# Performance work log

Hardware: AMD Instinct MI355X
Metric: run time of the kernel (lower is better)

The kernel has to match this reference:

```python
import jax, jax.numpy as jnp
import numpy as np

N_NODES = 100000
N_EDGES = 1600000
N_FEAT = 128
N_HID = 128


def cheb_conv_k2(x, edge_index, W0, W1, b):
    """PyG ChebConv with K=2, sym norm, lambda_max=2.0.
    Reduces to: out = x @ W0 + (L_hat x) @ W1 + b, where
    L_hat = 2L/lambda_max - I = -D^{-1/2} A D^{-1/2} (diagonal cancels).
    """
    n = x.shape[0]
    row, col = edge_index[0], edge_index[1]
    deg = jax.ops.segment_sum(jnp.ones_like(row, dtype=x.dtype), row, num_segments=n)
    dinv = jnp.where(deg > 0, jax.lax.rsqrt(jnp.maximum(deg, 1.0)), 0.0)
    w = -(dinv[row] * dinv[col])                     # [E] edge weights of L_hat
    tx1 = jax.ops.segment_sum(x[col] * w[:, None], row, num_segments=n)  # [N, F]
    return x @ W0 + tx1 @ W1 + b


def setup_inputs() -> dict:
    key = jax.random.key(0)
    ks = jax.random.split(key, 8)
    glorot = lambda k, fi, fo: jax.random.normal(k, (fi, fo), dtype=jnp.float32) * np.float32(np.sqrt(2.0 / (fi + fo)))
    x = jax.random.normal(ks[0], (N_NODES, N_FEAT), dtype=jnp.float32)
    edge_index = jax.random.randint(ks[1], (2, N_EDGES), 0, N_NODES, dtype=jnp.int64 if jax.config.jax_enable_x64 else jnp.int32)
    return {
        "x": x,
        "edge_index": edge_index,
        "W0_1": glorot(ks[2], N_FEAT, N_HID),
        "W1_1": glorot(ks[3], N_FEAT, N_HID),
        "b1": jnp.zeros((N_HID,), dtype=jnp.float32),
        "W0_2": glorot(ks[4], N_HID, N_HID),
        "W1_2": glorot(ks[5], N_HID, N_HID),
        "b2": jnp.zeros((N_HID,), dtype=jnp.float32),
    }


def reference(x, edge_index, W0_1, W1_1, b1, W0_2, W1_2, b2):
    # eval mode: input Dropout, dropout_adj(p=0.8), and per-layer Dropout are identity
    x1 = jax.nn.relu(cheb_conv_k2(x, edge_index, W0_1, W1_1, b1))
    x2 = jax.nn.relu(cheb_conv_k2(x1, edge_index, W0_2, W1_2, b2))
    # mean of the two layer outputs; outAct is identity
    return (x1 + x2) * 0.5
```

## Files before the change

### kernel.cpp

```cpp
#include <hip/hip_runtime.h>

#define NN 100000
#define NE 1600000
#define NF 128
#define NSTRIP2 (NN / 32)
#define NBUCK ((NN + 127) / 128)
#define CAP 2560
#define CHUNK 4096

typedef __attribute__((ext_vector_type(8))) short short8;
typedef __attribute__((ext_vector_type(4))) float f32x4;

__device__ __forceinline__ unsigned short f2b(float f) {
    union { float f; unsigned int u; } v; v.f = f;
    unsigned int u = v.u;
    unsigned int r = (u + 0x7fffu + ((u >> 16) & 1u)) >> 16;
    return (unsigned short)r;
}

__global__ __launch_bounds__(256) void k_bin(const int* __restrict__ row,
                                             const int* __restrict__ col,
                                             int* __restrict__ gcur,
                                             unsigned int* __restrict__ gslab) {
    __shared__ int hist[NBUCK];
    __shared__ int start[NBUCK];
    __shared__ int gbase[NBUCK];
    __shared__ int scanbuf[256];
    __shared__ unsigned int stage[CHUNK];
    __shared__ unsigned short sb[CHUNK];

    const int t = threadIdx.x;
    const int e0 = blockIdx.x * CHUNK;
    const int cnt = min(CHUNK, NE - e0);

    for (int i = t; i < NBUCK; i += 256) hist[i] = 0;
    __syncthreads();
    for (int i = t; i < cnt; i += 256) atomicAdd(&hist[row[e0 + i] >> 7], 1);
    __syncthreads();

    const int b0 = t * 4;
    int s = 0;
#pragma unroll
    for (int k = 0; k < 4; ++k) { int idx = b0 + k; if (idx < NBUCK) s += hist[idx]; }
    scanbuf[t] = s;
    __syncthreads();
    for (int off = 1; off < 256; off <<= 1) {
        int u = t >= off ? scanbuf[t - off] : 0;
        __syncthreads();
        scanbuf[t] += u;
        __syncthreads();
    }
    int run = t > 0 ? scanbuf[t - 1] : 0;
#pragma unroll
    for (int k = 0; k < 4; ++k) {
        int idx = b0 + k;
        if (idx < NBUCK) { start[idx] = run; run += hist[idx]; }
    }
    __syncthreads();

    for (int i = t; i < NBUCK; i += 256) {
        int c = hist[i];
        gbase[i] = c > 0 ? atomicAdd(&gcur[i], c) : 0;
        hist[i] = start[i];
    }
    __syncthreads();

    for (int i = t; i < cnt; i += 256) {
        int r = row[e0 + i];
        int b = r >> 7;
        int p = atomicAdd(&hist[b], 1);
        stage[p] = (unsigned int)col[e0 + i] | ((unsigned int)(r & 127) << 17);
        sb[p] = (unsigned short)b;
    }
    __syncthreads();

    for (int i = t; i < cnt; i += 256) {
        int b = sb[i];
        gslab[gbase[b] + (i - start[b])] = stage[i];
    }
}

__global__ __launch_bounds__(256) void k_bscan(const int* __restrict__ gcur,
                                               int* __restrict__ bbase) {
    __shared__ int s[NBUCK];
    int t = threadIdx.x;
    for (int i = t; i < NBUCK; i += 256) s[i] = gcur[i] - i * CAP;
    __syncthreads();
    if (t == 0) {
        int run = 0;
        for (int i = 0; i < NBUCK; ++i) { int v = s[i]; s[i] = run; run += v; }
    }
    __syncthreads();
    for (int i = t; i < NBUCK; i += 256) bbase[i] = s[i];
}

__global__ __launch_bounds__(256) void k_csr(const unsigned int* __restrict__ gslab,
                                             const int* __restrict__ gcur,
                                             const int* __restrict__ bbase,
                                             int* __restrict__ offs,
                                             int* __restrict__ ccol,
                                             float* __restrict__ dinv) {
    __shared__ int rh[128];
    __shared__ int rcur[128];
    __shared__ unsigned int scol[CAP];

    const int b = blockIdx.x;
    const int segbase = b * CAP;
    const int cnt = gcur[b] - segbase;
    const int csr0 = bbase[b];
    const int t = threadIdx.x;

    if (t < 128) rh[t] = 0;
    __syncthreads();
    for (int i = t; i < cnt; i += 256) atomicAdd(&rh[gslab[segbase + i] >> 17], 1);
    __syncthreads();
    if (t == 0) {
        int run = 0;
        for (int r = 0; r < 128; ++r) { rcur[r] = run; run += rh[r]; }
    }
    __syncthreads();

    const int rbase = b * 128;
    if (t < 128 && rbase + t < NN) {
        offs[rbase + t] = csr0 + rcur[t];
        int d = rh[t];
        dinv[rbase + t] = d > 0 ? rsqrtf((float)d) : 0.0f;
    }
    if (b == NBUCK - 1 && t == 0) offs[NN] = NE;
    __syncthreads();

    for (int i = t; i < cnt; i += 256) {
        unsigned int v = gslab[segbase + i];
        int p = atomicAdd(&rcur[v >> 17], 1);
        scol[p] = v & 0x1ffff;
    }
    __syncthreads();
    for (int i = t; i < cnt; i += 256) ccol[csr0 + i] = scol[i];
}

__global__ __launch_bounds__(256) void k_quant(const float* __restrict__ x,
                                               const float* __restrict__ dinv,
                                               unsigned short* __restrict__ xq,
                                               float* __restrict__ dsc,
                                               float* __restrict__ sx) {
    int r = (blockIdx.x * 256 + threadIdx.x) >> 6;
    int lane = threadIdx.x & 63;
    float2 v = ((const float2*)x)[r * 64 + lane];
    float m = fmaxf(fabsf(v.x), fabsf(v.y));
#pragma unroll
    for (int mask = 32; mask; mask >>= 1) m = fmaxf(m, __shfl_xor(m, mask));
    float s = m * (1.0f / 127.0f);
    float inv = m > 0.0f ? 127.0f / m : 0.0f;
    int qx = (int)rintf(v.x * inv) + 128;
    int qy = (int)rintf(v.y * inv) + 128;
    xq[r * 64 + lane] = (unsigned short)(qx | (qy << 8));
    if (lane == 0) { dsc[r] = dinv[r] * s; sx[r] = s; }
}

__global__ __launch_bounds__(256) void k_pack(const float* __restrict__ W01,
                                              const float* __restrict__ W11,
                                              const float* __restrict__ W02,
                                              const float* __restrict__ W12,
                                              unsigned short* __restrict__ WP,
                                              int* __restrict__ gcur) {
    int idx = blockIdx.x * 256 + threadIdx.x;
    if (idx < NBUCK) gcur[idx] = idx * CAP;
    int mi = idx >> 14;
    int e = idx & 16383;
    const float* W = mi == 0 ? W01 : mi == 1 ? W02 : mi == 2 ? W11 : W12;
    int midx = mi == 0 ? 0 : mi == 1 ? 2 : mi == 2 ? 1 : 3;
    int k = e >> 7, n = e & 127;
    int kt = k >> 5, g = (k >> 3) & 3, j = k & 7;
    WP[midx * 16384 + (((kt * 4 + g) * 128 + n) << 3) + j] = f2b(W[e]);
}

__global__ __launch_bounds__(256) void k_gather(const int* __restrict__ offs,
                                                const int* __restrict__ ccol,
                                                const float* __restrict__ dsc,
                                                const float* __restrict__ dinv,
                                                const uint2* __restrict__ xq64,
                                                uint2* __restrict__ txq8,
                                                float* __restrict__ st_out,
                                                float qbias) {
    int r = (blockIdx.x * 256 + threadIdx.x) >> 6;
    if (r >= NN) return;
    int lane = threadIdx.x & 63;
    int fl = lane & 15, q = lane >> 4;
    int beg = offs[r], end = offs[r + 1];
    float a0 = 0.f, a1 = 0.f, a2 = 0.f, a3 = 0.f;
    float a4 = 0.f, a5 = 0.f, a6 = 0.f, a7 = 0.f, S = 0.f;
    int j = beg + q;
    for (; j + 12 < end; j += 16) {
        int c0 = ccol[j], c1 = ccol[j + 4], c2 = ccol[j + 8], c3 = ccol[j + 12];
        float w0 = dsc[c0], w1 = dsc[c1], w2 = dsc[c2], w3 = dsc[c3];
        uint2 u0 = xq64[c0 * 16 + fl];
        uint2 u1 = xq64[c1 * 16 + fl];
        uint2 u2 = xq64[c2 * 16 + fl];
        uint2 u3 = xq64[c3 * 16 + fl];
        a0 += w0 * (float)(u0.x & 0xffu)         + w1 * (float)(u1.x & 0xffu)
            + w2 * (float)(u2.x & 0xffu)         + w3 * (float)(u3.x & 0xffu);
        a1 += w0 * (float)((u0.x >> 8) & 0xffu)  + w1 * (float)((u1.x >> 8) & 0xffu)
            + w2 * (float)((u2.x >> 8) & 0xffu)  + w3 * (float)((u3.x >> 8) & 0xffu);
        a2 += w0 * (float)((u0.x >> 16) & 0xffu) + w1 * (float)((u1.x >> 16) & 0xffu)
            + w2 * (float)((u2.x >> 16) & 0xffu) + w3 * (float)((u3.x >> 16) & 0xffu);
        a3 += w0 * (float)(u0.x >> 24)           + w1 * (float)(u1.x >> 24)
            + w2 * (float)(u2.x >> 24)           + w3 * (float)(u3.x >> 24);
        a4 += w0 * (float)(u0.y & 0xffu)         + w1 * (float)(u1.y & 0xffu)
            + w2 * (float)(u2.y & 0xffu)         + w3 * (float)(u3.y & 0xffu);
        a5 += w0 * (float)((u0.y >> 8) & 0xffu)  + w1 * (float)((u1.y >> 8) & 0xffu)
            + w2 * (float)((u2.y >> 8) & 0xffu)  + w3 * (float)((u3.y >> 8) & 0xffu);
        a6 += w0 * (float)((u0.y >> 16) & 0xffu) + w1 * (float)((u1.y >> 16) & 0xffu)
            + w2 * (float)((u2.y >> 16) & 0xffu) + w3 * (float)((u3.y >> 16) & 0xffu);
        a7 += w0 * (float)(u0.y >> 24)           + w1 * (float)(u1.y >> 24)
            + w2 * (float)(u2.y >> 24)           + w3 * (float)(u3.y >> 24);
        S += w0 + w1 + w2 + w3;
    }
    for (; j < end; j += 4) {
        int c = ccol[j];
        float w = dsc[c];
        uint2 u = xq64[c * 16 + fl];
        a0 += w * (float)(u.x & 0xffu);
        a1 += w * (float)((u.x >> 8) & 0xffu);
        a2 += w * (float)((u.x >> 16) & 0xffu);
        a3 += w * (float)(u.x >> 24);
        a4 += w * (float)(u.y & 0xffu);
        a5 += w * (float)((u.y >> 8) & 0xffu);
        a6 += w * (float)((u.y >> 16) & 0xffu);
        a7 += w * (float)(u.y >> 24);
        S += w;
    }
#pragma unroll
    for (int mask = 32; mask >= 16; mask >>= 1) {
        a0 += __shfl_xor(a0, mask); a1 += __shfl_xor(a1, mask);
        a2 += __shfl_xor(a2, mask); a3 += __shfl_xor(a3, mask);
        a4 += __shfl_xor(a4, mask); a5 += __shfl_xor(a5, mask);
        a6 += __shfl_xor(a6, mask); a7 += __shfl_xor(a7, mask);
        S  += __shfl_xor(S, mask);
    }
    if (q == 0) {
        float s = -dinv[r];
        float qb = qbias * S;
        a0 = s * (a0 - qb); a1 = s * (a1 - qb); a2 = s * (a2 - qb); a3 = s * (a3 - qb);
        a4 = s * (a4 - qb); a5 = s * (a5 - qb); a6 = s * (a6 - qb); a7 = s * (a7 - qb);
        float mx = fmaxf(fmaxf(fmaxf(fabsf(a0), fabsf(a1)), fmaxf(fabsf(a2), fabsf(a3))),
                         fmaxf(fmaxf(fabsf(a4), fabsf(a5)), fmaxf(fabsf(a6), fabsf(a7))));
#pragma unroll
        for (int mask = 8; mask; mask >>= 1) mx = fmaxf(mx, __shfl_xor(mx, mask));
        float st = mx * (1.0f / 127.0f);
        float invt = mx > 0.0f ? 127.0f / mx : 0.0f;
        int q0 = (int)rintf(a0 * invt) + 128, q1 = (int)rintf(a1 * invt) + 128;
        int q2 = (int)rintf(a2 * invt) + 128, q3 = (int)rintf(a3 * invt) + 128;
        int q4 = (int)rintf(a4 * invt) + 128, q5 = (int)rintf(a5 * invt) + 128;
        int q6 = (int)rintf(a6 * invt) + 128, q7 = (int)rintf(a7 * invt) + 128;
        uint2 o;
        o.x = (unsigned)q0 | ((unsigned)q1 << 8) | ((unsigned)q2 << 16) | ((unsigned)q3 << 24);
        o.y = (unsigned)q4 | ((unsigned)q5 << 8) | ((unsigned)q6 << 16) | ((unsigned)q7 << 24);
        txq8[r * 16 + fl] = o;
        if (fl == 0) st_out[r] = st;
    }
}

__global__ __launch_bounds__(256) void k_mm(const unsigned char* __restrict__ Aq,
                                            const float* __restrict__ s_in,
                                            float qoff,
                                            const unsigned char* __restrict__ Tq8,
                                            const float* __restrict__ st_in,
                                            const unsigned short* __restrict__ WP0,
                                            const unsigned short* __restrict__ WP1,
                                            const float* __restrict__ bias,
                                            const float* __restrict__ dinv,
                                            float* __restrict__ out,
                                            unsigned char* __restrict__ Qout,
                                            float* __restrict__ dsc_out,
                                            float* __restrict__ s1_out,
                                            int mode) {
    int wid = (blockIdx.x * 256 + threadIdx.x) >> 6;
    if (wid >= NSTRIP2) return;
    int lane = threadIdx.x & 63;
    int g = lane >> 4, m = lane & 15;

    short8 a[2][4], t[2][4];
#pragma unroll
    for (int s = 0; s < 2; ++s) {
        int row = wid * 32 + s * 16 + m;
        float sA = s_in[row];
        float sT = st_in[row];
        const unsigned char* Arow = Aq + (size_t)row * NF + g * 8;
        const unsigned char* Trow = Tq8 + (size_t)row * NF + g * 8;
#pragma unroll
        for (int kt = 0; kt < 4; ++kt) {
            uint2 u = *(const uint2*)(Arow + kt * 32);
            short8 v;
            v[0] = f2b(sA * ((float)(u.x & 0xffu) - qoff));
            v[1] = f2b(sA * ((float)((u.x >> 8) & 0xffu) - qoff));
            v[2] = f2b(sA * ((float)((u.x >> 16) & 0xffu) - qoff));
            v[3] = f2b(sA * ((float)(u.x >> 24) - qoff));
            v[4] = f2b(sA * ((float)(u.y & 0xffu) - qoff));
            v[5] = f2b(sA * ((float)((u.y >> 8) & 0xffu) - qoff));
            v[6] = f2b(sA * ((float)((u.y >> 16) & 0xffu) - qoff));
            v[7] = f2b(sA * ((float)(u.y >> 24) - qoff));
            a[s][kt] = v;
            uint2 w = *(const uint2*)(Trow + kt * 32);
            short8 tv;
            tv[0] = f2b(sT * ((float)(w.x & 0xffu) - 128.0f));
            tv[1] = f2b(sT * ((float)((w.x >> 8) & 0xffu) - 128.0f));
            tv[2] = f2b(sT * ((float)((w.x >> 16) & 0xffu) - 128.0f));
            tv[3] = f2b(sT * ((float)(w.x >> 24) - 128.0f));
            tv[4] = f2b(sT * ((float)(w.y & 0xffu) - 128.0f));
            tv[5] = f2b(sT * ((float)((w.y >> 8) & 0xffu) - 128.0f));
            tv[6] = f2b(sT * ((float)((w.y >> 16) & 0xffu) - 128.0f));
            tv[7] = f2b(sT * ((float)(w.y >> 24) - 128.0f));
            t[s][kt] = tv;
        }
    }

    const short8* B0 = (const short8*)WP0 + g * 128 + m;
    const short8* B1 = (const short8*)WP1 + g * 128 + m;

    f32x4 acc[2][8];
#pragma unroll
    for (int nt = 0; nt < 8; ++nt) {
        float b = bias[nt * 16 + m];
#pragma unroll
        for (int s = 0; s < 2; ++s) {
            acc[s][nt][0] = b; acc[s][nt][1] = b; acc[s][nt][2] = b; acc[s][nt][3] = b;
        }
    }

#pragma unroll
    for (int nt = 0; nt < 8; ++nt) {
#pragma unroll
        for (int kt = 0; kt < 4; ++kt) {
            short8 b0 = B0[kt * 512 + nt * 16];
            short8 b1 = B1[kt * 512 + nt * 16];
#pragma unroll
            for (int s = 0; s < 2; ++s) {
                acc[s][nt] = __builtin_amdgcn_mfma_f32_16x16x32_bf16(a[s][kt], b0, acc[s][nt], 0, 0, 0);
                acc[s][nt] = __builtin_amdgcn_mfma_f32_16x16x32_bf16(t[s][kt], b1, acc[s][nt], 0, 0, 0);
            }
        }
    }

#pragma unroll
    for (int s = 0; s < 2; ++s)
#pragma unroll
        for (int nt = 0; nt < 8; ++nt)
#pragma unroll
            for (int r = 0; r < 4; ++r) acc[s][nt][r] = fmaxf(acc[s][nt][r], 0.0f);

    if (mode == 0) {
#pragma unroll
        for (int s = 0; s < 2; ++s) {
            int rbase = wid * 32 + s * 16 + g * 4;
            float mr[4] = {0.0f, 0.0f, 0.0f, 0.0f};
#pragma unroll
            for (int nt = 0; nt < 8; ++nt)
#pragma unroll
                for (int r = 0; r < 4; ++r) mr[r] = fmaxf(mr[r], acc[s][nt][r]);
#pragma unroll
            for (int mask = 1; mask < 16; mask <<= 1)
#pragma unroll
                for (int r = 0; r < 4; ++r) mr[r] = fmaxf(mr[r], __shfl_xor(mr[r], mask));

            float inv[4], s1v[4];
#pragma unroll
            for (int r = 0; r < 4; ++r) {
                s1v[r] = mr[r] * (1.0f / 255.0f);
                inv[r] = mr[r] > 0.0f ? 255.0f / mr[r] : 0.0f;
            }
#pragma unroll
            for (int nt = 0; nt < 8; ++nt) {
                int c = nt * 16 + m;
#pragma unroll
                for (int r = 0; r < 4; ++r) {
                    int qv = (int)rintf(acc[s][nt][r] * inv[r]);
                    qv = qv > 255 ? 255 : qv;
                    Qout[(size_t)(rbase + r) * NF + c] = (unsigned char)qv;
                }
            }
            if (m == 0) {
#pragma unroll
                for (int r = 0; r < 4; ++r) {
                    s1_out[rbase + r] = s1v[r];
                    dsc_out[rbase + r] = dinv[rbase + r] * s1v[r];
                }
            }
        }
    } else {
#pragma unroll
        for (int s = 0; s < 2; ++s) {
            int rbase = wid * 32 + s * 16 + g * 4;
            float sR[4];
#pragma unroll
            for (int r = 0; r < 4; ++r) sR[r] = s_in[rbase + r];
#pragma unroll
            for (int nt = 0; nt < 8; ++nt) {
                int c = nt * 16 + m;
#pragma unroll
                for (int r = 0; r < 4; ++r) {
                    size_t o = (size_t)(rbase + r) * NF + c;
                    float x1v = sR[r] * (float)Aq[o];
                    out[o] = 0.5f * (x1v + acc[s][nt][r]);
                }
            }
        }
    }
}

extern "C" void kernel_launch(void* const* d_in, const int* in_sizes, int n_in,
                              void* d_out, int out_size, void* d_ws, size_t ws_size,
                              hipStream_t stream) {
    const float* x   = (const float*)d_in[0];
    const int*   ei  = (const int*)d_in[1];
    const float* W01 = (const float*)d_in[2];
    const float* W11 = (const float*)d_in[3];
    const float* b1  = (const float*)d_in[4];
    const float* W02 = (const float*)d_in[5];
    const float* W12 = (const float*)d_in[6];
    const float* b2  = (const float*)d_in[7];
    float* out = (float*)d_out;

    const int* row = ei;
    const int* col = ei + NE;

    char* ws = (char*)d_ws;
    int*            gcur  = (int*)(ws);
    int*            bbase = (int*)(ws + 3200);
    float*          dinv  = (float*)(ws + 6400);
    int*            offs  = (int*)(ws + 406400);
    int*            ccol  = (int*)(ws + 806416);
    unsigned short* WP    = (unsigned short*)(ws + 7206416);
    float*          dsc   = (float*)(ws + 7337488);
    float*          s1a   = (float*)(ws + 7737488);
    float*          sx    = (float*)(ws + 8137488);
    float*          st    = (float*)(ws + 8537488);
    unsigned short* xq    = (unsigned short*)(ws + 8937488);
    unsigned char*  txq   = (unsigned char*)(ws + 21737488);
    unsigned int*   gslab = (unsigned int*)(ws + 21737488);

    unsigned char*  xq8 = (unsigned char*)xq;
    unsigned short* WP01 = WP;
    unsigned short* WP11 = WP + 16384;
    unsigned short* WP02 = WP + 32768;
    unsigned short* WP12 = WP + 49152;

    k_pack <<<(4 * 16384) / 256, 256, 0, stream>>>(W01, W11, W02, W12, WP, gcur);
    k_bin  <<<(NE + CHUNK - 1) / CHUNK, 256, 0, stream>>>(row, col, gcur, gslab);
    k_bscan<<<1, 256, 0, stream>>>(gcur, bbase);
    k_csr  <<<NBUCK, 256, 0, stream>>>(gslab, gcur, bbase, offs, ccol, dinv);

    k_quant<<<(NN * 64) / 256, 256, 0, stream>>>(x, dinv, xq, dsc, sx);

    const int gatherBlocks = (NN * 64) / 256;
    const int mmBlocks = (NSTRIP2 * 64 + 255) / 256;

    k_gather<<<gatherBlocks, 256, 0, stream>>>(offs, ccol, dsc, dinv,
                                               (const uint2*)xq, (uint2*)txq, st, 128.0f);
    k_mm    <<<mmBlocks, 256, 0, stream>>>(xq8, sx, 128.0f, txq, st,
                                           WP01, WP11, b1, dinv, out, xq8, dsc, s1a, 0);

    k_gather<<<gatherBlocks, 256, 0, stream>>>(offs, ccol, dsc, dinv,
                                               (const uint2*)xq, (uint2*)txq, st, 0.0f);
    k_mm    <<<mmBlocks, 256, 0, stream>>>(xq8, s1a, 0.0f, txq, st,
                                           WP02, WP12, b2, dinv, out, xq8, dsc, s1a, 1);
}
```

Measured before the change: 251.1 us.

## Store aggregated features as bf16 instead of int8 and enlarge binning chunks

The gather kernel now writes its aggregated features directly as bf16, dropping the per-row absmax reduction, int8 quantization and scale array. The matmul kernel loads bf16 fragments directly instead of dequantizing int8. This removes compute and a side array but doubles the bytes written and read for the intermediate. Separately, the binning kernel uses 512 threads and 8192-edge chunks, which halves the number of blocks and the global atomics on the bucket cursors.

```diff
diff --git a/kernel.cpp b/kernel.cpp
--- a/kernel.cpp
+++ b/kernel.cpp
@@ -6,7 +6,7 @@
 #define NSTRIP2 (NN / 32)
 #define NBUCK ((NN + 127) / 128)
 #define CAP 2560
-#define CHUNK 4096
+#define CHUNK 8192
 
 typedef __attribute__((ext_vector_type(8))) short short8;
 typedef __attribute__((ext_vector_type(4))) float f32x4;
@@ -18,14 +18,14 @@
     return (unsigned short)r;
 }
 
-__global__ __launch_bounds__(256) void k_bin(const int* __restrict__ row,
+__global__ __launch_bounds__(512) void k_bin(const int* __restrict__ row,
                                              const int* __restrict__ col,
                                              int* __restrict__ gcur,
                                              unsigned int* __restrict__ gslab) {
     __shared__ int hist[NBUCK];
     __shared__ int start[NBUCK];
     __shared__ int gbase[NBUCK];
-    __shared__ int scanbuf[256];
+    __shared__ int scanbuf[512];
     __shared__ unsigned int stage[CHUNK];
     __shared__ unsigned short sb[CHUNK];
 
@@ -33,18 +33,18 @@
     const int e0 = blockIdx.x * CHUNK;
     const int cnt = min(CHUNK, NE - e0);
 
-    for (int i = t; i < NBUCK; i += 256) hist[i] = 0;
-    __syncthreads();
-    for (int i = t; i < cnt; i += 256) atomicAdd(&hist[row[e0 + i] >> 7], 1);
-    __syncthreads();
-
-    const int b0 = t * 4;
+    for (int i = t; i < NBUCK; i += 512) hist[i] = 0;
+    __syncthreads();
+    for (int i = t; i < cnt; i += 512) atomicAdd(&hist[row[e0 + i] >> 7], 1);
+    __syncthreads();
+
+    const int b0 = t * 2;
     int s = 0;
 #pragma unroll
-    for (int k = 0; k < 4; ++k) { int idx = b0 + k; if (idx < NBUCK) s += hist[idx]; }
+    for (int k = 0; k < 2; ++k) { int idx = b0 + k; if (idx < NBUCK) s += hist[idx]; }
     scanbuf[t] = s;
     __syncthreads();
-    for (int off = 1; off < 256; off <<= 1) {
+    for (int off = 1; off < 512; off <<= 1) {
         int u = t >= off ? scanbuf[t - off] : 0;
         __syncthreads();
         scanbuf[t] += u;
@@ -52,20 +52,20 @@
     }
     int run = t > 0 ? scanbuf[t - 1] : 0;
 #pragma unroll
-    for (int k = 0; k < 4; ++k) {
+    for (int k = 0; k < 2; ++k) {
         int idx = b0 + k;
         if (idx < NBUCK) { start[idx] = run; run += hist[idx]; }
     }
     __syncthreads();
 
-    for (int i = t; i < NBUCK; i += 256) {
+    for (int i = t; i < NBUCK; i += 512) {
         int c = hist[i];
         gbase[i] = c > 0 ? atomicAdd(&gcur[i], c) : 0;
         hist[i] = start[i];
     }
     __syncthreads();
 
-    for (int i = t; i < cnt; i += 256) {
+    for (int i = t; i < cnt; i += 512) {
         int r = row[e0 + i];
         int b = r >> 7;
         int p = atomicAdd(&hist[b], 1);
@@ -74,7 +74,7 @@
     }
     __syncthreads();
 
-    for (int i = t; i < cnt; i += 256) {
+    for (int i = t; i < cnt; i += 512) {
         int b = sb[i];
         gslab[gbase[b] + (i - start[b])] = stage[i];
     }
@@ -179,8 +179,7 @@
                                                 const float* __restrict__ dsc,
                                                 const float* __restrict__ dinv,
                                                 const uint2* __restrict__ xq64,
-                                                uint2* __restrict__ txq8,
-                                                float* __restrict__ st_out,
+                                                uint4* __restrict__ txb4,
                                                 float qbias) {
     int r = (blockIdx.x * 256 + threadIdx.x) >> 6;
     if (r >= NN) return;
@@ -242,29 +241,19 @@
         float qb = qbias * S;
         a0 = s * (a0 - qb); a1 = s * (a1 - qb); a2 = s * (a2 - qb); a3 = s * (a3 - qb);
         a4 = s * (a4 - qb); a5 = s * (a5 - qb); a6 = s * (a6 - qb); a7 = s * (a7 - qb);
-        float mx = fmaxf(fmaxf(fmaxf(fabsf(a0), fabsf(a1)), fmaxf(fabsf(a2), fabsf(a3))),
-                         fmaxf(fmaxf(fabsf(a4), fabsf(a5)), fmaxf(fabsf(a6), fabsf(a7))));
-#pragma unroll
-        for (int mask = 8; mask; mask >>= 1) mx = fmaxf(mx, __shfl_xor(mx, mask));
-        float st = mx * (1.0f / 127.0f);
-        float invt = mx > 0.0f ? 127.0f / mx : 0.0f;
-        int q0 = (int)rintf(a0 * invt) + 128, q1 = (int)rintf(a1 * invt) + 128;
-        int q2 = (int)rintf(a2 * invt) + 128, q3 = (int)rintf(a3 * invt) + 128;
-        int q4 = (int)rintf(a4 * invt) + 128, q5 = (int)rintf(a5 * invt) + 128;
-        int q6 = (int)rintf(a6 * invt) + 128, q7 = (int)rintf(a7 * invt) + 128;
-        uint2 o;
-        o.x = (unsigned)q0 | ((unsigned)q1 << 8) | ((unsigned)q2 << 16) | ((unsigned)q3 << 24);
-        o.y = (unsigned)q4 | ((unsigned)q5 << 8) | ((unsigned)q6 << 16) | ((unsigned)q7 << 24);
-        txq8[r * 16 + fl] = o;
-        if (fl == 0) st_out[r] = st;
+        uint4 o;
+        o.x = (unsigned int)f2b(a0) | ((unsigned int)f2b(a1) << 16);
+        o.y = (unsigned int)f2b(a2) | ((unsigned int)f2b(a3) << 16);
+        o.z = (unsigned int)f2b(a4) | ((unsigned int)f2b(a5) << 16);
+        o.w = (unsigned int)f2b(a6) | ((unsigned int)f2b(a7) << 16);
+        txb4[r * 16 + fl] = o;
     }
 }
 
 __global__ __launch_bounds__(256) void k_mm(const unsigned char* __restrict__ Aq,
                                             const float* __restrict__ s_in,
                                             float qoff,
-                                            const unsigned char* __restrict__ Tq8,
-                                            const float* __restrict__ st_in,
+                                            const unsigned short* __restrict__ Tbf,
                                             const unsigned short* __restrict__ WP0,
                                             const unsigned short* __restrict__ WP1,
                                             const float* __restrict__ bias,
@@ -284,9 +273,8 @@
     for (int s = 0; s < 2; ++s) {
         int row = wid * 32 + s * 16 + m;
         float sA = s_in[row];
-        float sT = st_in[row];
         const unsigned char* Arow = Aq + (size_t)row * NF + g * 8;
-        const unsigned char* Trow = Tq8 + (size_t)row * NF + g * 8;
+        const short8* Tfr = (const short8*)(Tbf + (size_t)row * NF + g * 8);
 #pragma unroll
         for (int kt = 0; kt < 4; ++kt) {
             uint2 u = *(const uint2*)(Arow + kt * 32);
@@ -300,17 +288,7 @@
             v[6] = f2b(sA * ((float)((u.y >> 16) & 0xffu) - qoff));
             v[7] = f2b(sA * ((float)(u.y >> 24) - qoff));
             a[s][kt] = v;
-            uint2 w = *(const uint2*)(Trow + kt * 32);
-            short8 tv;
-            tv[0] = f2b(sT * ((float)(w.x & 0xffu) - 128.0f));
-            tv[1] = f2b(sT * ((float)((w.x >> 8) & 0xffu) - 128.0f));
-            tv[2] = f2b(sT * ((float)((w.x >> 16) & 0xffu) - 128.0f));
-            tv[3] = f2b(sT * ((float)(w.x >> 24) - 128.0f));
-            tv[4] = f2b(sT * ((float)(w.y & 0xffu) - 128.0f));
-            tv[5] = f2b(sT * ((float)((w.y >> 8) & 0xffu) - 128.0f));
-            tv[6] = f2b(sT * ((float)((w.y >> 16) & 0xffu) - 128.0f));
-            tv[7] = f2b(sT * ((float)(w.y >> 24) - 128.0f));
-            t[s][kt] = tv;
+            t[s][kt] = Tfr[kt * 4];
         }
     }
 
@@ -433,10 +411,9 @@
     float*          dsc   = (float*)(ws + 7337488);
     float*          s1a   = (float*)(ws + 7737488);
     float*          sx    = (float*)(ws + 8137488);
-    float*          st    = (float*)(ws + 8537488);
-    unsigned short* xq    = (unsigned short*)(ws + 8937488);
-    unsigned char*  txq   = (unsigned char*)(ws + 21737488);
-    unsigned int*   gslab = (unsigned int*)(ws + 21737488);
+    unsigned short* xq    = (unsigned short*)(ws + 8537488);
+    unsigned int*   txb   = (unsigned int*)(ws + 21337488);
+    unsigned int*   gslab = (unsigned int*)(ws + 21337488);
 
     unsigned char*  xq8 = (unsigned char*)xq;
     unsigned short* WP01 = WP;
@@ -445,7 +422,7 @@
     unsigned short* WP12 = WP + 49152;
 
     k_pack <<<(4 * 16384) / 256, 256, 0, stream>>>(W01, W11, W02, W12, WP, gcur);
-    k_bin  <<<(NE + CHUNK - 1) / CHUNK, 256, 0, stream>>>(row, col, gcur, gslab);
+    k_bin  <<<(NE + CHUNK - 1) / CHUNK, 512, 0, stream>>>(row, col, gcur, gslab);
     k_bscan<<<1, 256, 0, stream>>>(gcur, bbase);
     k_csr  <<<NBUCK, 256, 0, stream>>>(gslab, gcur, bbase, offs, ccol, dinv);
 
@@ -455,12 +432,12 @@
     const int mmBlocks = (NSTRIP2 * 64 + 255) / 256;
 
     k_gather<<<gatherBlocks, 256, 0, stream>>>(offs, ccol, dsc, dinv,
-                                               (const uint2*)xq, (uint2*)txq, st, 128.0f);
-    k_mm    <<<mmBlocks, 256, 0, stream>>>(xq8, sx, 128.0f, txq, st,
+                                               (const uint2*)xq, (uint4*)txb, 128.0f);
+    k_mm    <<<mmBlocks, 256, 0, stream>>>(xq8, sx, 128.0f, (const unsigned short*)txb,
                                            WP01, WP11, b1, dinv, out, xq8, dsc, s1a, 0);
 
     k_gather<<<gatherBlocks, 256, 0, stream>>>(offs, ccol, dsc, dinv,
-                                               (const uint2*)xq, (uint2*)txq, st, 0.0f);
-    k_mm    <<<mmBlocks, 256, 0, stream>>>(xq8, s1a, 0.0f, txq, st,
+                                               (const uint2*)xq, (uint4*)txb, 0.0f);
+    k_mm    <<<mmBlocks, 256, 0, stream>>>(xq8, s1a, 0.0f, (const unsigned short*)txb,
                                            WP02, WP12, b2, dinv, out, xq8, dsc, s1a, 1);
 }
```

Result: faster. 239.1 us (-4.8%).
